# Kernel tuning notes

Measured on AMD Instinct MI355X. Metric: run time of the kernel, lower is better.

## Reference

```python
import jax, jax.numpy as jnp
import numpy as np

P = 7  # corr_size
P2 = P * P
NEG_SLOPE = 0.01  # default LeakyReLU


def _correlate(f1, f2):
    """spatial_correlation_sample with kernel_size=1, stride=1, padding=0,
    dilation_patch=1: out[b,pi,pj,y,x] = sum_c f1[b,c,y,x] * f2[b,c,y+pi-r,x+pj-r]
    (zero padded), returned flattened to [b, P*P, h, w]."""
    r = P // 2
    b, c, h, w = f1.shape
    f2p = jnp.pad(f2, ((0, 0), (0, 0), (r, r), (r, r)))
    outs = []
    for pi in range(P):
        for pj in range(P):
            sh = jax.lax.slice(f2p, (0, 0, pi, pj), (b, c, pi + h, pj + w))
            outs.append(jnp.sum(f1 * sh, axis=1))  # [b,h,w]
    return jnp.stack(outs, axis=1)  # [b, P*P, h, w]


def _conv3x3(x, w, b):
    y = jax.lax.conv_general_dilated(
        x, w, window_strides=(1, 1), padding=((1, 1), (1, 1)),
        dimension_numbers=('NCHW', 'OIHW', 'NCHW'))
    return y + b[None, :, None, None]


def _up_nearest(x, s):
    return jnp.repeat(jnp.repeat(x, s, axis=2), s, axis=3)


def _level(feat1, feat2, h_pre, c_pre, w, b, scale):
    # feat1 = current frame (x), feat2 = previous frame (x_pre)
    u1 = _up_nearest(feat1, scale)
    u2 = _up_nearest(feat2, scale)
    corr = _correlate(u1, u2)                        # [B, P*P, H*s, W*s]
    corr = jnp.where(corr >= 0, corr, NEG_SLOPE * corr)  # leaky relu
    dw = corr[:, :, ::scale, ::scale]                # nearest downsample back
    lstm_in = jnp.concatenate([dw, h_pre], axis=1)   # [B, 2*P*P, H, W]
    conv = _conv3x3(lstm_in, w, b)                   # [B, 4*P*P, H, W]
    cc_i, cc_f, cc_o, cc_g = jnp.split(conv, 4, axis=1)
    i = jax.nn.sigmoid(cc_i)
    f = jax.nn.sigmoid(cc_f)
    o = jax.nn.sigmoid(cc_o)
    g = jnp.tanh(cc_g)
    c_next = f * c_pre + i * g
    h_next = o * jnp.tanh(c_next)
    return h_next, c_next


def setup_inputs() -> dict:
    key = jax.random.key(0)
    ks = jax.random.split(key, 10)
    x0 = jax.random.normal(ks[0], (2, 512, 64, 64), jnp.float32) * 0.1
    x1 = jax.random.normal(ks[1], (2, 1024, 32, 32), jnp.float32) * 0.1
    xp0 = jax.random.normal(ks[2], (2, 512, 64, 64), jnp.float32) * 0.1
    xp1 = jax.random.normal(ks[3], (2, 1024, 32, 32), jnp.float32) * 0.1
    h0 = jax.random.normal(ks[4], (2, P2, 64, 64), jnp.float32) * 0.1
    c0 = jax.random.normal(ks[5], (2, P2, 64, 64), jnp.float32) * 0.1
    h1 = jax.random.normal(ks[6], (2, P2, 32, 32), jnp.float32) * 0.1
    c1 = jax.random.normal(ks[7], (2, P2, 32, 32), jnp.float32) * 0.1
    w0 = jax.random.normal(ks[8], (4 * P2, 2 * P2, 3, 3), jnp.float32) * 0.02
    w1 = jax.random.normal(ks[9], (4 * P2, 2 * P2, 3, 3), jnp.float32) * 0.02
    # init_weights sets the forget-gate bias slice to 1
    b0 = jnp.zeros((4 * P2,), jnp.float32).at[P2:2 * P2].set(1.0)
    b1 = jnp.zeros((4 * P2,), jnp.float32).at[P2:2 * P2].set(1.0)
    return {"x0": x0, "x1": x1, "xp0": xp0, "xp1": xp1,
            "h0": h0, "c0": c0, "h1": h1, "c1": c1,
            "w0": w0, "b0": b0, "w1": w1, "b1": b1}


def reference(x0, x1, xp0, xp1, h0, c0, h1, c1, w0, b0, w1, b1):
    # level i: upsample scale = upsample_param * 2**i = 2 * 2**i
    h0n, c0n = _level(x0, xp0, h0, c0, w0, b0, scale=2)
    h1n, c1n = _level(x1, xp1, h1, c1, w1, b1, scale=4)
    return (h0n, c0n, h1n, c1n)
```

## Files before the change

### kernel.cpp

```cpp
#include <hip/hip_runtime.h>

#define DEVFN __device__ __forceinline__

typedef __attribute__((ext_vector_type(8))) __bf16 bf16x8;
typedef __attribute__((ext_vector_type(16))) float f32x16;
typedef unsigned short ushort;

DEVFN float sigmoidf_(float x) { return 1.f / (1.f + __expf(-x)); }

DEVFN ushort f2bf(float f) {
    unsigned u = __float_as_uint(f);
    unsigned r = (u + 0x7FFF + ((u >> 16) & 1)) >> 16;
    return (ushort)r;
}

template<int C, int CHUNK, int CH, int H, int W, int TW, int TH, int NOFF, int OFS>
__global__ void corr_kernel(const float* __restrict__ f1, const float* __restrict__ f2,
                            float* __restrict__ accout) {
    const int HW = H * W;
    const int FW = TW + NOFF - 1;
    const int FH = TH + NOFF - 1;
    __shared__ float f2s[CH][FH * FW];
    const int y0    = blockIdx.x * TH;
    const int b     = blockIdx.y;
    const int chunk = blockIdx.z;
    const int t  = threadIdx.x;
    const int tx = t % TW;
    const int ty = t / TW;

    float acc[NOFF][NOFF];
#pragma unroll
    for (int i = 0; i < NOFF; ++i)
#pragma unroll
        for (int jj = 0; jj < NOFF; ++jj) acc[i][jj] = 0.f;

    const float* f1b = f1 + ((size_t)b * C + (size_t)chunk * CHUNK) * HW;
    const float* f2b = f2 + ((size_t)b * C + (size_t)chunk * CHUNK) * HW;
    const int myoff = (y0 + ty) * W + tx;

#pragma unroll 1
    for (int c0 = 0; c0 < CHUNK; c0 += CH) {
        __syncthreads();
        for (int e = t; e < CH * FH * FW; e += TW * TH) {
            int ch = e / (FH * FW);
            int e2 = e - ch * (FH * FW);
            int r  = e2 / FW, cc = e2 - r * FW;
            int gy = y0 - OFS + r;
            int gx = cc - OFS;
            float v = 0.f;
            if (gy >= 0 && gy < H && gx >= 0 && gx < W) v = f2b[(size_t)(c0 + ch) * HW + gy * W + gx];
            f2s[ch][e2] = v;
        }
        __syncthreads();
#pragma unroll
        for (int ch = 0; ch < CH; ++ch) {
            float f1v = f1b[(size_t)(c0 + ch) * HW + myoff];
#pragma unroll
            for (int dyi = 0; dyi < NOFF; ++dyi)
#pragma unroll
                for (int dxi = 0; dxi < NOFF; ++dxi)
                    acc[dyi][dxi] = fmaf(f1v, f2s[ch][(ty + dyi) * FW + tx + dxi], acc[dyi][dxi]);
        }
    }

    float* ao = accout + ((size_t)b * NOFF * NOFF) * HW + myoff;
#pragma unroll
    for (int dyi = 0; dyi < NOFF; ++dyi)
#pragma unroll
        for (int dxi = 0; dxi < NOFF; ++dxi)
            atomicAdd(&ao[(size_t)(dyi * NOFF + dxi) * HW], acc[dyi][dxi]);
}

template<int H, int W, int SCALE, int SHIFT, int NOFF, int OFS>
__global__ void xbuild_kernel(const float* __restrict__ corr_acc, const float* __restrict__ h_pre,
                              ushort* __restrict__ Xin) {
    const int HW = H * W;
    int i = blockIdx.x * 256 + threadIdx.x;
    if (i >= 2 * HW * 16) return;
    int g  = i & 15;
    int px = (i >> 4) % HW;
    int b  = (i >> 4) / HW;
    int y = px / W, x = px - y * W;
    ushort out8[8];
#pragma unroll
    for (int j = 0; j < 8; ++j) {
        int ic = g * 8 + j;
        float v = 0.f;
        if (ic < 49) {
            int pi = ic / 7, pj = ic - pi * 7;
            int dy = pi - 3, dx = pj - 3;
            int uy = SCALE * y + dy, ux = SCALE * x + dx;
            if (uy >= 0 && uy < SCALE * H && ux >= 0 && ux < SCALE * W) {
                int idy = (dy >> SHIFT) + OFS;
                int idx = (dx >> SHIFT) + OFS;
                float cv = corr_acc[((size_t)b * NOFF * NOFF + idy * NOFF + idx) * HW + px];
                v = cv >= 0.f ? cv : 0.01f * cv;
            }
        } else if (ic < 98) {
            v = h_pre[((size_t)b * 49 + (ic - 49)) * HW + px];
        }
        out8[j] = f2bf(v);
    }
    *reinterpret_cast<uint4*>(Xin + (size_t)i * 8) = *reinterpret_cast<uint4*>(out8);
}

__global__ void wprep_kernel(const float* __restrict__ w, ushort* __restrict__ Wmf) {
    int i = blockIdx.x * 256 + threadIdx.x;
    const int n = 9 * 16 * 256 * 8;
    if (i >= n) return;
    int iEl = i & 7;
    int oc  = (i >> 3) & 255;
    int icg = (i >> 11) & 15;
    int tap = i >> 15;
    int ic  = icg * 8 + iEl;
    float v = (oc < 196 && ic < 98) ? w[((size_t)oc * 98 + ic) * 9 + tap] : 0.f;
    Wmf[i] = f2bf(v);
}

template<int H, int W, int SPLIT, int ICPS, int NKC, int STRIDE>
__global__ void convmf_kernel(const ushort* __restrict__ Xin, const ushort* __restrict__ Wmf,
                              float* __restrict__ Y) {
    const int HW = H * W;
    __shared__ ushort Xs[180 * STRIDE];
    const int tilesx = W / 16;
    const int by0 = (blockIdx.x / tilesx) * 8;
    const int bx0 = (blockIdx.x % tilesx) * 16;
    const int ocb = blockIdx.y * 64;
    const int b   = blockIdx.z & 1;
    const int s   = blockIdx.z >> 1;
    const int t   = threadIdx.x;
    const int wv  = t >> 6;
    const int l   = t & 63;
    const int G   = ICPS / 8;

    for (int u = t; u < 180 * G; u += 256) {
        int px = u / G, g = u - px * G;
        int gy = by0 + px / 18 - 1;
        int gx = bx0 + px % 18 - 1;
        uint4 v = make_uint4(0u, 0u, 0u, 0u);
        if (gy >= 0 && gy < H && gx >= 0 && gx < W)
            v = *reinterpret_cast<const uint4*>(Xin + (((size_t)b * HW + gy * W + gx) * 128 + s * ICPS + g * 8));
        *reinterpret_cast<uint4*>(&Xs[px * STRIDE + g * 8]) = v;
    }
    __syncthreads();

    f32x16 acc0 = {};
    f32x16 acc1 = {};
    const int n    = l & 31;
    const int hi   = l >> 5;
    const int wrow = 2 * wv + (n >> 4);
    const int wcol = n & 15;

#pragma unroll 1
    for (int kc = 0; kc < NKC; ++kc) {
        bf16x8 af[2][9];
        const int icg = (s * ICPS + kc * 16) / 8 + hi;
        const ushort* wp = Wmf + ((size_t)icg * 256 + ocb + n) * 8;
#pragma unroll
        for (int j = 0; j < 9; ++j) {
            af[0][j] = *reinterpret_cast<const bf16x8*>(wp + (size_t)j * 16 * 256 * 8);
            af[1][j] = *reinterpret_cast<const bf16x8*>(wp + (size_t)j * 16 * 256 * 8 + 32 * 8);
        }
#pragma unroll
        for (int j = 0; j < 9; ++j) {
            const int ky = j / 3, kx = j - (j / 3) * 3;
            const int hp = (wrow + ky) * 18 + wcol + kx;
            bf16x8 bf = *reinterpret_cast<const bf16x8*>(&Xs[hp * STRIDE + kc * 16 + hi * 8]);
            acc0 = __builtin_amdgcn_mfma_f32_32x32x16_bf16(af[0][j], bf, acc0, 0, 0, 0);
            acc1 = __builtin_amdgcn_mfma_f32_32x32x16_bf16(af[1][j], bf, acc1, 0, 0, 0);
        }
    }

    float* Yo = Y + ((size_t)(s * 2 + b) * 196) * HW;
    const int po = (by0 + wrow) * W + bx0 + wcol;
#pragma unroll
    for (int r = 0; r < 16; ++r) {
        int m = (r & 3) + 8 * (r >> 2) + 4 * hi;
        int oc0 = ocb + m;
        if (oc0 < 196) Yo[(size_t)oc0 * HW + po] = acc0[r];
        int oc1 = ocb + 32 + m;
        if (oc1 < 196) Yo[(size_t)oc1 * HW + po] = acc1[r];
    }
}

template<int S, int HW>
__global__ void lstm_kernel(const float* __restrict__ Y, const float* __restrict__ bias,
                            const float* __restrict__ c_pre,
                            float* __restrict__ h_out, float* __restrict__ c_out) {
    int i = blockIdx.x * 256 + threadIdx.x;
    const int n = 2 * 49 * HW;
    if (i >= n) return;
    int b   = i / (49 * HW);
    int rem = i - b * (49 * HW);
    int k   = rem / HW;
    float g4[4];
#pragma unroll
    for (int gi = 0; gi < 4; ++gi) {
        float v = bias[gi * 49 + k];
#pragma unroll
        for (int ss = 0; ss < S; ++ss)
            v += Y[((size_t)((ss * 2 + b) * 196) + gi * 49) * HW + rem];
        g4[gi] = v;
    }
    float iv = sigmoidf_(g4[0]);
    float fv = sigmoidf_(g4[1]);
    float ov = sigmoidf_(g4[2]);
    float gv = tanhf(g4[3]);
    float cp = c_pre[i];
    float cn = fv * cp + iv * gv;
    h_out[i] = ov * tanhf(cn);
    c_out[i] = cn;
}

extern "C" void kernel_launch(void* const* d_in, const int* in_sizes, int n_in,
                              void* d_out, int out_size, void* d_ws, size_t ws_size,
                              hipStream_t stream) {
    (void)in_sizes; (void)n_in; (void)out_size; (void)ws_size;
    const float* x0  = (const float*)d_in[0];
    const float* x1  = (const float*)d_in[1];
    const float* xp0 = (const float*)d_in[2];
    const float* xp1 = (const float*)d_in[3];
    const float* h0  = (const float*)d_in[4];
    const float* c0  = (const float*)d_in[5];
    const float* h1  = (const float*)d_in[6];
    const float* c1  = (const float*)d_in[7];
    const float* w0  = (const float*)d_in[8];
    const float* b0  = (const float*)d_in[9];
    const float* w1  = (const float*)d_in[10];
    const float* b1  = (const float*)d_in[11];
    float* out = (float*)d_out;

    float* ws = (float*)d_ws;
    float*  Wmf0f  = ws;
    float*  Wmf1f  = Wmf0f + 147456;
    float*  accC0  = Wmf1f + 147456;
    float*  accC1  = accC0 + 131072;
    float*  Xin0f  = accC1 + 8192;
    float*  Xin1f  = Xin0f + 524288;
    float*  Y0     = Xin1f + 131072;
    float*  Y1     = Y0 + 3211264;
    ushort* Wmf0 = (ushort*)Wmf0f;
    ushort* Wmf1 = (ushort*)Wmf1f;
    ushort* Xin0 = (ushort*)Xin0f;
    ushort* Xin1 = (ushort*)Xin1f;

    hipMemsetAsync(accC0, 0, (size_t)(131072 + 8192) * sizeof(float), stream);

    wprep_kernel<<<1152, 256, 0, stream>>>(w0, Wmf0);
    wprep_kernel<<<1152, 256, 0, stream>>>(w1, Wmf1);

    corr_kernel<512, 32, 8, 64, 64, 64, 4, 4, 2><<<dim3(16, 2, 16), 256, 0, stream>>>(x0, xp0, accC0);
    corr_kernel<1024, 64, 16, 32, 32, 32, 8, 2, 1><<<dim3(4, 2, 16), 256, 0, stream>>>(x1, xp1, accC1);

    xbuild_kernel<64, 64, 2, 1, 4, 2><<<512, 256, 0, stream>>>(accC0, h0, Xin0);
    xbuild_kernel<32, 32, 4, 2, 2, 1><<<128, 256, 0, stream>>>(accC1, h1, Xin1);

    convmf_kernel<64, 64, 2, 64, 4, 72><<<dim3(32, 4, 4), 256, 0, stream>>>(Xin0, Wmf0, Y0);
    convmf_kernel<32, 32, 4, 32, 2, 40><<<dim3(8, 4, 8), 256, 0, stream>>>(Xin1, Wmf1, Y1);

    lstm_kernel<2, 4096><<<1568, 256, 0, stream>>>(Y0, b0, c0, out + 0,      out + 401408);
    lstm_kernel<4, 1024><<<392,  256, 0, stream>>>(Y1, b1, c1, out + 802816, out + 903168);
}
```

Measured before the change: 230.1 us.

## Rewrite correlation kernel with per-thread 4-pixel register tiles and sliced atomic accumulation

```diff
diff --git a/kernel.cpp b/kernel.cpp
--- a/kernel.cpp
+++ b/kernel.cpp
@@ -14,64 +14,68 @@
     return (ushort)r;
 }
 
-template<int C, int CHUNK, int CH, int H, int W, int TW, int TH, int NOFF, int OFS>
+template<int C, int CC, int H, int W, int NOFF, int OFS, int NSLICE, int UNR>
 __global__ void corr_kernel(const float* __restrict__ f1, const float* __restrict__ f2,
                             float* __restrict__ accout) {
-    const int HW = H * W;
-    const int FW = TW + NOFF - 1;
-    const int FH = TH + NOFF - 1;
-    __shared__ float f2s[CH][FH * FW];
-    const int y0    = blockIdx.x * TH;
+    constexpr int HW = H * W;
+    constexpr bool NEEDHI = (NOFF - 1 - OFS) >= 1;
+    const int t     = threadIdx.x;
+    const int px    = blockIdx.x * 1024 + t * 4;
     const int b     = blockIdx.y;
     const int chunk = blockIdx.z;
-    const int t  = threadIdx.x;
-    const int tx = t % TW;
-    const int ty = t / TW;
-
-    float acc[NOFF][NOFF];
+    const int y  = px / W;
+    const int x0 = px - y * W;
+
+    const float* f1p = f1 + ((size_t)b * C + chunk * CC) * HW + px;
+    const float* f2b = f2 + ((size_t)b * C + chunk * CC) * HW;
+
+    float acc[NOFF][NOFF][4];
 #pragma unroll
     for (int i = 0; i < NOFF; ++i)
 #pragma unroll
-        for (int jj = 0; jj < NOFF; ++jj) acc[i][jj] = 0.f;
-
-    const float* f1b = f1 + ((size_t)b * C + (size_t)chunk * CHUNK) * HW;
-    const float* f2b = f2 + ((size_t)b * C + (size_t)chunk * CHUNK) * HW;
-    const int myoff = (y0 + ty) * W + tx;
-
-#pragma unroll 1
-    for (int c0 = 0; c0 < CHUNK; c0 += CH) {
-        __syncthreads();
-        for (int e = t; e < CH * FH * FW; e += TW * TH) {
-            int ch = e / (FH * FW);
-            int e2 = e - ch * (FH * FW);
-            int r  = e2 / FW, cc = e2 - r * FW;
-            int gy = y0 - OFS + r;
-            int gx = cc - OFS;
-            float v = 0.f;
-            if (gy >= 0 && gy < H && gx >= 0 && gx < W) v = f2b[(size_t)(c0 + ch) * HW + gy * W + gx];
-            f2s[ch][e2] = v;
-        }
-        __syncthreads();
-#pragma unroll
-        for (int ch = 0; ch < CH; ++ch) {
-            float f1v = f1b[(size_t)(c0 + ch) * HW + myoff];
-#pragma unroll
-            for (int dyi = 0; dyi < NOFF; ++dyi)
-#pragma unroll
-                for (int dxi = 0; dxi < NOFF; ++dxi)
-                    acc[dyi][dxi] = fmaf(f1v, f2s[ch][(ty + dyi) * FW + tx + dxi], acc[dyi][dxi]);
-        }
-    }
-
-    float* ao = accout + ((size_t)b * NOFF * NOFF) * HW + myoff;
+        for (int j = 0; j < NOFF; ++j)
+#pragma unroll
+            for (int p = 0; p < 4; ++p) acc[i][j][p] = 0.f;
+
+#pragma unroll UNR
+    for (int c = 0; c < CC; ++c) {
+        float f1a[4];
+        *reinterpret_cast<float4*>(f1a) = *reinterpret_cast<const float4*>(f1p + (size_t)c * HW);
+        const float* f2c = f2b + (size_t)c * HW;
+#pragma unroll
+        for (int dyi = 0; dyi < NOFF; ++dyi) {
+            const int yy = y + dyi - OFS;
+            const bool rv = (yy >= 0) && (yy < H);
+            const float* rp = f2c + yy * W + x0;
+            float w[12];
+            float4 z = make_float4(0.f, 0.f, 0.f, 0.f);
+            float4 lo  = (rv && x0 >= 4)    ? *reinterpret_cast<const float4*>(rp - 4) : z;
+            float4 mid = rv                 ? *reinterpret_cast<const float4*>(rp)     : z;
+            float4 hi  = (NEEDHI && rv && (x0 + 4 < W)) ? *reinterpret_cast<const float4*>(rp + 4) : z;
+            *reinterpret_cast<float4*>(&w[0]) = lo;
+            *reinterpret_cast<float4*>(&w[4]) = mid;
+            *reinterpret_cast<float4*>(&w[8]) = hi;
+#pragma unroll
+            for (int dxi = 0; dxi < NOFF; ++dxi)
+#pragma unroll
+                for (int p = 0; p < 4; ++p)
+                    acc[dyi][dxi][p] = fmaf(f1a[p], w[4 + p + dxi - OFS], acc[dyi][dxi][p]);
+        }
+    }
+
+    const int slice = chunk & (NSLICE - 1);
+    float* ao = accout + ((size_t)(slice * 2 + b) * NOFF * NOFF) * HW + px;
 #pragma unroll
     for (int dyi = 0; dyi < NOFF; ++dyi)
 #pragma unroll
-        for (int dxi = 0; dxi < NOFF; ++dxi)
-            atomicAdd(&ao[(size_t)(dyi * NOFF + dxi) * HW], acc[dyi][dxi]);
-}
-
-template<int H, int W, int SCALE, int SHIFT, int NOFF, int OFS>
+        for (int dxi = 0; dxi < NOFF; ++dxi) {
+            float* p4 = ao + (size_t)(dyi * NOFF + dxi) * HW;
+#pragma unroll
+            for (int p = 0; p < 4; ++p) atomicAdd(p4 + p, acc[dyi][dxi][p]);
+        }
+}
+
+template<int H, int W, int SCALE, int SHIFT, int NOFF, int OFS, int NSLICE>
 __global__ void xbuild_kernel(const float* __restrict__ corr_acc, const float* __restrict__ h_pre,
                               ushort* __restrict__ Xin) {
     const int HW = H * W;
@@ -93,7 +97,10 @@
             if (uy >= 0 && uy < SCALE * H && ux >= 0 && ux < SCALE * W) {
                 int idy = (dy >> SHIFT) + OFS;
                 int idx = (dx >> SHIFT) + OFS;
-                float cv = corr_acc[((size_t)b * NOFF * NOFF + idy * NOFF + idx) * HW + px];
+                float cv = 0.f;
+#pragma unroll
+                for (int s = 0; s < NSLICE; ++s)
+                    cv += corr_acc[((size_t)(s * 2 + b) * NOFF * NOFF + idy * NOFF + idx) * HW + px];
                 v = cv >= 0.f ? cv : 0.01f * cv;
             }
         } else if (ic < 98) {
@@ -104,7 +111,10 @@
     *reinterpret_cast<uint4*>(Xin + (size_t)i * 8) = *reinterpret_cast<uint4*>(out8);
 }
 
-__global__ void wprep_kernel(const float* __restrict__ w, ushort* __restrict__ Wmf) {
+__global__ void wprep_kernel(const float* __restrict__ w0, const float* __restrict__ w1,
+                             ushort* __restrict__ Wmf0, ushort* __restrict__ Wmf1) {
+    const float* w = blockIdx.y ? w1 : w0;
+    ushort* Wmf    = blockIdx.y ? Wmf1 : Wmf0;
     int i = blockIdx.x * 256 + threadIdx.x;
     const int n = 9 * 16 * 256 * 8;
     if (i >= n) return;
@@ -231,29 +241,28 @@
     float* out = (float*)d_out;
 
     float* ws = (float*)d_ws;
-    float*  Wmf0f  = ws;
-    float*  Wmf1f  = Wmf0f + 147456;
-    float*  accC0  = Wmf1f + 147456;
-    float*  accC1  = accC0 + 131072;
-    float*  Xin0f  = accC1 + 8192;
-    float*  Xin1f  = Xin0f + 524288;
-    float*  Y0     = Xin1f + 131072;
-    float*  Y1     = Y0 + 3211264;
+    float*  Wmf0f = ws;
+    float*  Wmf1f = Wmf0f + 147456;
+    float*  Xin0f = Wmf1f + 147456;
+    float*  Xin1f = Xin0f + 524288;
+    float*  Y0    = Xin1f + 131072;
+    float*  Y1    = Y0 + 3211264;
+    float*  accC0s = Y0;
+    float*  accC1s = Y0 + 524288;
     ushort* Wmf0 = (ushort*)Wmf0f;
     ushort* Wmf1 = (ushort*)Wmf1f;
     ushort* Xin0 = (ushort*)Xin0f;
     ushort* Xin1 = (ushort*)Xin1f;
 
-    hipMemsetAsync(accC0, 0, (size_t)(131072 + 8192) * sizeof(float), stream);
-
-    wprep_kernel<<<1152, 256, 0, stream>>>(w0, Wmf0);
-    wprep_kernel<<<1152, 256, 0, stream>>>(w1, Wmf1);
-
-    corr_kernel<512, 32, 8, 64, 64, 64, 4, 4, 2><<<dim3(16, 2, 16), 256, 0, stream>>>(x0, xp0, accC0);
-    corr_kernel<1024, 64, 16, 32, 32, 32, 8, 2, 1><<<dim3(4, 2, 16), 256, 0, stream>>>(x1, xp1, accC1);
-
-    xbuild_kernel<64, 64, 2, 1, 4, 2><<<512, 256, 0, stream>>>(accC0, h0, Xin0);
-    xbuild_kernel<32, 32, 4, 2, 2, 1><<<128, 256, 0, stream>>>(accC1, h1, Xin1);
+    hipMemsetAsync(accC0s, 0, (size_t)(524288 + 32768) * sizeof(float), stream);
+
+    wprep_kernel<<<dim3(1152, 2), 256, 0, stream>>>(w0, w1, Wmf0, Wmf1);
+
+    corr_kernel<512, 8, 64, 64, 4, 2, 4, 2><<<dim3(4, 2, 64), 256, 0, stream>>>(x0, xp0, accC0s);
+    corr_kernel<1024, 8, 32, 32, 2, 1, 4, 4><<<dim3(1, 2, 128), 256, 0, stream>>>(x1, xp1, accC1s);
+
+    xbuild_kernel<64, 64, 2, 1, 4, 2, 4><<<512, 256, 0, stream>>>(accC0s, h0, Xin0);
+    xbuild_kernel<32, 32, 4, 2, 2, 1, 4><<<128, 256, 0, stream>>>(accC1s, h1, Xin1);
 
     convmf_kernel<64, 64, 2, 64, 4, 72><<<dim3(32, 4, 4), 256, 0, stream>>>(Xin0, Wmf0, Y0);
     convmf_kernel<32, 32, 4, 32, 2, 40><<<dim3(8, 4, 8), 256, 0, stream>>>(Xin1, Wmf1, Y1);
```

Result: slower. 294.9 us (+28.1%).
